# Kernel tuning notes

Hardware: AMD Instinct MI355X
Metric: run time of the kernel (lower is better)

Reference implementation:

```python
import jax, jax.numpy as jnp
import numpy as np

NUM_CLASSES = 80
STRIDES = (8, 16, 32)


def _decode(p, stride):
    # p: [B, 5+C, H, W] raw head -> [B, HW, 5+C] decoded (xy in px, wh=exp*stride)
    B, C, H, W = p.shape
    ys, xs = jnp.meshgrid(jnp.arange(H), jnp.arange(W), indexing='ij')
    grid = jnp.stack([xs, ys], -1).reshape(H * W, 2).astype(p.dtype)
    out = p.reshape(B, C, H * W).transpose(0, 2, 1)
    xy = (out[..., :2] + grid) * stride
    wh = jnp.exp(out[..., 2:4]) * stride
    out = jnp.concatenate([xy, wh, out[..., 4:]], -1)
    es = jnp.full((H * W,), float(stride), p.dtype)
    return out, grid[:, 0], grid[:, 1], es


def _pairwise_iou(gt, pr):
    # gt [G,4] cxcywh, pr [A,4] -> [G,A]
    gt_tl = gt[:, None, :2] - gt[:, None, 2:] * 0.5
    gt_br = gt[:, None, :2] + gt[:, None, 2:] * 0.5
    pr_tl = pr[None, :, :2] - pr[None, :, 2:] * 0.5
    pr_br = pr[None, :, :2] + pr[None, :, 2:] * 0.5
    tl = jnp.maximum(gt_tl, pr_tl)
    br = jnp.minimum(gt_br, pr_br)
    en = jnp.all(tl < br, -1).astype(gt.dtype)
    inter = jnp.prod(br - tl, -1) * en
    a_gt = jnp.prod(gt[:, 2:], -1)[:, None]
    a_pr = jnp.prod(pr[:, 2:], -1)[None, :]
    return inter / (a_gt + a_pr - inter + 1e-16)


def _assign(gt_boxes, gt_cls, bbox, clsp, objp, xg, yg, es):
    # SimOTA assignment for one image (all fixed-shape; non-candidate anchors
    # are masked out via huge cost instead of boolean gather).
    G = gt_boxes.shape[0]
    xc = (xg + 0.5) * es  # [A] anchor centers
    yc = (yg + 0.5) * es
    gl = gt_boxes[:, 0:1] - 0.5 * gt_boxes[:, 2:3]
    gr = gt_boxes[:, 0:1] + 0.5 * gt_boxes[:, 2:3]
    gt_ = gt_boxes[:, 1:2] - 0.5 * gt_boxes[:, 3:4]
    gb = gt_boxes[:, 1:2] + 0.5 * gt_boxes[:, 3:4]
    in_box = (xc[None] > gl) & (xc[None] < gr) & (yc[None] > gt_) & (yc[None] < gb)  # [G,A]
    r = 2.5 * es[None]
    in_ctr = ((xc[None] > gt_boxes[:, 0:1] - r) & (xc[None] < gt_boxes[:, 0:1] + r)
              & (yc[None] > gt_boxes[:, 1:2] - r) & (yc[None] < gt_boxes[:, 1:2] + r))
    fg_cand = jnp.any(in_box, 0) | jnp.any(in_ctr, 0)  # [A]
    in_both = in_box & in_ctr  # [G,A]

    ious = _pairwise_iou(gt_boxes, bbox)  # [G,A]
    ious_m = jnp.where(fg_cand[None, :], ious, 0.0)
    iou_cost = -jnp.log(ious_m + 1e-8)

    # pairwise cls BCE cost: bce(sqrt(sigmoid(cls)*sigmoid(obj)), onehot(gt)).sum(-1)
    p = jnp.sqrt(jax.nn.sigmoid(clsp) * jax.nn.sigmoid(objp[:, None]))  # [A,C]
    lp = jnp.maximum(jnp.log(p), -100.0)
    l1p = jnp.maximum(jnp.log1p(-p), -100.0)
    t = jax.nn.one_hot(gt_cls, NUM_CLASSES, dtype=p.dtype)  # [G,C]
    cls_cost = -(jnp.einsum('ac,gc->ga', lp - l1p, t) + jnp.sum(l1p, -1)[None, :])

    cost = (cls_cost + 3.0 * iou_cost
            + 1e5 * (~in_both).astype(p.dtype)
            + 1e9 * (~fg_cand)[None, :].astype(p.dtype))

    # dynamic-k: k_g = clamp(sum(top10 ious), min=1)
    topk_ious, _ = jax.lax.top_k(ious_m, 10)
    dyn_k = jnp.clip(topk_ious.sum(-1).astype(jnp.int32), 1, None)  # [G]
    rank = jnp.argsort(jnp.argsort(cost, axis=1), axis=1)  # rank of each anchor per gt
    matching = (rank < dyn_k[:, None]) & fg_cand[None, :]  # [G,A]
    # resolve anchors matched to multiple gts: keep min-cost gt
    multi = matching.sum(0) > 1
    best = jnp.argmin(cost, 0)
    matching = jnp.where(multi[None, :], jnp.arange(G)[:, None] == best[None, :], matching)

    fg = jnp.any(matching, 0)  # [A]
    matched_gt = jnp.argmax(matching, 0)  # [A]
    pred_iou = jnp.sum(matching * ious, 0)  # [A]
    matched_cls = gt_cls[matched_gt]
    return fg, matched_gt, pred_iou, matched_cls


def _giou_loss(b, g):
    tl = jnp.maximum(b[..., :2] - b[..., 2:] * 0.5, g[..., :2] - g[..., 2:] * 0.5)
    br = jnp.minimum(b[..., :2] + b[..., 2:] * 0.5, g[..., :2] + g[..., 2:] * 0.5)
    area_b = jnp.prod(b[..., 2:], -1)
    area_g = jnp.prod(g[..., 2:], -1)
    en = jnp.all(tl < br, -1).astype(b.dtype)
    inter = jnp.prod(br - tl, -1) * en
    union = area_b + area_g - inter
    iou = inter / (union + 1e-16)
    ctl = jnp.minimum(b[..., :2] - b[..., 2:] * 0.5, g[..., :2] - g[..., 2:] * 0.5)
    cbr = jnp.maximum(b[..., :2] + b[..., 2:] * 0.5, g[..., :2] + g[..., 2:] * 0.5)
    area_c = jnp.maximum(jnp.prod(cbr - ctl, -1), 1e-16)
    giou = iou - (area_c - union) / area_c
    return 1.0 - jnp.clip(giou, -1.0, 1.0)


def _bce_logits(x, t):
    return jnp.maximum(x, 0.0) - x * t + jnp.log1p(jnp.exp(-jnp.abs(x)))


def _forward(p8, p16, p32, labels):
    outs, xo, yo, eo = [], [], [], []
    for p, s in zip((p8, p16, p32), STRIDES):
        o, x, y, e = _decode(p, s)
        outs.append(o); xo.append(x); yo.append(y); eo.append(e)
    outputs = jnp.concatenate(outs, 1)  # [B, A, 5+C]
    xg = jnp.concatenate(xo); yg = jnp.concatenate(yo); es = jnp.concatenate(eo)

    bbox = outputs[..., :4]
    obj = outputs[..., 4]
    cls = outputs[..., 5:]
    gt_boxes = labels[..., :4]
    gt_cls = labels[..., 4].astype(jnp.int32)

    # assignment runs under no_grad in torch
    det = jax.lax.stop_gradient(outputs)
    fg, matched_gt, pred_iou, matched_cls = jax.vmap(
        lambda gb, gc, o: _assign(gb, gc, o[..., :4], o[..., 5:], o[..., 4], xg, yg, es)
    )(gt_boxes, gt_cls, det)

    fgf = fg.astype(outputs.dtype)  # [B,A]
    reg_t = jnp.take_along_axis(gt_boxes, matched_gt[..., None], axis=1)  # [B,A,4]
    cls_t = (jax.nn.one_hot(matched_cls, NUM_CLASSES, dtype=outputs.dtype)
             * pred_iou[..., None] * fgf[..., None])

    loss_iou = jnp.sum(_giou_loss(bbox, reg_t) * fgf)
    loss_obj = jnp.sum(_bce_logits(obj, fgf))
    loss_cls = jnp.sum(_bce_logits(cls, cls_t) * fgf[..., None])
    num_fg = jnp.maximum(jnp.sum(fgf), 1.0)
    return (5.0 * loss_iou + loss_obj + loss_cls) / num_fg


def setup_inputs() -> dict:
    key = jax.random.key(0)
    k1, k2, k3, k4, k5, k6 = jax.random.split(key, 6)
    B, NGT = 32, 20
    p8 = jax.random.normal(k1, (B, 5 + NUM_CLASSES, 80, 80), dtype=jnp.float32)
    p16 = jax.random.normal(k2, (B, 5 + NUM_CLASSES, 40, 40), dtype=jnp.float32)
    p32 = jax.random.normal(k3, (B, 5 + NUM_CLASSES, 20, 20), dtype=jnp.float32)
    cxy = jax.random.uniform(k4, (B, NGT, 2), dtype=jnp.float32, minval=32.0, maxval=608.0)
    wh = jax.random.uniform(k5, (B, NGT, 2), dtype=jnp.float32, minval=16.0, maxval=128.0)
    cls = jax.random.randint(k6, (B, NGT, 1), 0, NUM_CLASSES).astype(jnp.float32)
    labels = jnp.concatenate([cxy, wh, cls], -1)
    return {"p8": p8, "p16": p16, "p32": p32, "labels": labels}


def reference(p8, p16, p32, labels):
    return _forward(p8, p16, p32, labels)
```

## Files before the change

kernel.cpp:

```cpp
#include <hip/hip_runtime.h>
#include <cstdint>
#include <cstddef>

#define NA 8400
#define NAP 8448
#define NB 32
#define NG 20
#define NCL 80
#define NBLK 33

__device__ __forceinline__ float frcp(float x) { return __builtin_amdgcn_rcpf(x); }
__device__ __forceinline__ float bce0(float x) {
  return fmaxf(x, 0.0f) + __logf(1.0f + __expf(-fabsf(x)));
}

__device__ __forceinline__ void anchor_info(int a, const float* p8, const float* p16,
                                            const float* p32, int b, const float*& base,
                                            int& hw, int& HW, int& xg, int& yg, float& fs) {
  if (a < 6400)      { hw = a;        HW = 6400; xg = hw % 80; yg = hw / 80; fs = 8.f;
                       base = p8  + (size_t)b * 85 * 6400; }
  else if (a < 8000) { hw = a - 6400; HW = 1600; xg = hw % 40; yg = hw / 40; fs = 16.f;
                       base = p16 + (size_t)b * 85 * 1600; }
  else               { hw = a - 8000; HW = 400;  xg = hw % 20; yg = hw / 20; fs = 32.f;
                       base = p32 + (size_t)b * 85 * 400; }
}

__device__ __forceinline__ float iou_raw(float gx, float gy, float gw, float gh, float4 p) {
  float gtlx = gx - gw * 0.5f, gtly = gy - gh * 0.5f;
  float gbrx = gx + gw * 0.5f, gbry = gy + gh * 0.5f;
  float ptlx = p.x - p.z * 0.5f, ptly = p.y - p.w * 0.5f;
  float pbrx = p.x + p.z * 0.5f, pbry = p.y + p.w * 0.5f;
  float tlx = fmaxf(gtlx, ptlx), tly = fmaxf(gtly, ptly);
  float brx = fminf(gbrx, pbrx), bry = fminf(gbry, pbry);
  float inter = ((tlx < brx) && (tly < bry)) ? (brx - tlx) * (bry - tly) : 0.0f;
  float ag = gw * gh, ap = p.z * p.w;
  return inter * frcp(ag + ap - inter + 1e-16f);
}

__device__ __forceinline__ float cost_for(float gx, float gy, float gw, float gh, int cg,
                                          int g, unsigned int am, float lso, float slr,
                                          const float* base, int hw, int HW, float4 pb,
                                          float& iou_out) {
  float x = base[(size_t)(5 + cg) * HW + hw];
  float u = __logf(1.0f + __expf(-fabsf(x)));
  float lsx = fminf(x, 0.0f) - u;
  float lpr = 0.5f * (lsx + lso);
  float p   = __expf(lpr);
  float l1p = fmaxf(__logf(1.0f - p), -100.0f);
  float wv  = fmaxf(lpr, -100.0f) - l1p;
  float iou = iou_raw(gx, gy, gw, gh, pb);
  iou_out = iou;
  float cst = -(wv + slr) - 3.0f * __logf(iou + 1e-8f);
  if (!((am >> g) & 1u)) cst += 100000.0f;
  return cst;
}

__device__ __forceinline__ float giou_loss(float4 bb, float gx, float gy, float gw, float gh) {
  float btlx = bb.x - bb.z * 0.5f, btly = bb.y - bb.w * 0.5f;
  float bbrx = bb.x + bb.z * 0.5f, bbry = bb.y + bb.w * 0.5f;
  float gtlx = gx - gw * 0.5f, gtly = gy - gh * 0.5f;
  float gbrx = gx + gw * 0.5f, gbry = gy + gh * 0.5f;
  float tlx = fmaxf(btlx, gtlx), tly = fmaxf(btly, gtly);
  float brx = fminf(bbrx, gbrx), bry = fminf(bbry, gbry);
  float area_b = bb.z * bb.w, area_g = gw * gh;
  float inter = ((tlx < brx) && (tly < bry)) ? (brx - tlx) * (bry - tly) : 0.0f;
  float uni = area_b + area_g - inter;
  float iou = inter / (uni + 1e-16f);
  float ctlx = fminf(btlx, gtlx), ctly = fminf(btly, gtly);
  float cbrx = fmaxf(bbrx, gbrx), cbry = fmaxf(bbry, gbry);
  float area_c = fmaxf((cbrx - ctlx) * (cbry - ctly), 1e-16f);
  float giou = iou - (area_c - uni) / area_c;
  giou = fminf(fmaxf(giou, -1.0f), 1.0f);
  return 1.0f - giou;
}

__global__ __launch_bounds__(256) void kA(const float* __restrict__ p8,
                                          const float* __restrict__ p16,
                                          const float* __restrict__ p32,
                                          const float* __restrict__ labels,
                                          int* __restrict__ n_fg_cnt,
                                          float4* __restrict__ meta_c,
                                          float4* __restrict__ bbox_c,
                                          float* __restrict__ sb_c,
                                          unsigned int* __restrict__ match_c,
                                          float* __restrict__ blk_obj) {
  __shared__ float s_gt[NG * 4];
  __shared__ int   s_a[256];
  __shared__ unsigned int s_m[256];
  __shared__ float s_lso[256];
  __shared__ float s_sl[8][33];
  __shared__ float s_sbv[8][33];
  __shared__ unsigned int s_wcnt[4];
  __shared__ float s_part[4];
  __shared__ unsigned int s_base;
  __shared__ int s_cnt;

  int blk = blockIdx.x, b = blockIdx.y, tid = threadIdx.x, lane = tid & 63, wid = tid >> 6;
  size_t bo = (size_t)b * NAP;

  if (tid < NG) {
    s_gt[tid * 4 + 0] = labels[((size_t)b * NG + tid) * 5 + 0];
    s_gt[tid * 4 + 1] = labels[((size_t)b * NG + tid) * 5 + 1];
    s_gt[tid * 4 + 2] = labels[((size_t)b * NG + tid) * 5 + 2];
    s_gt[tid * 4 + 3] = labels[((size_t)b * NG + tid) * 5 + 3];
  }
  __syncthreads();

  int a = blk * 256 + tid;
  match_c[bo + a] = 0u;
  bool fg = false;
  unsigned int msk = 0u;
  float bce_obj = 0.0f, obj = 0.0f;
  const float* base = nullptr; int hw = 0, HW = 0, xg = 0, yg = 0; float fs = 8.f;
  if (a < NA) {
    anchor_info(a, p8, p16, p32, b, base, hw, HW, xg, yg, fs);
    obj = base[4 * HW + hw];
    bce_obj = bce0(obj);
    float xc = ((float)xg + 0.5f) * fs;
    float yc = ((float)yg + 0.5f) * fs;
    float r = 2.5f * fs;
#pragma unroll
    for (int g = 0; g < NG; ++g) {
      float gx = s_gt[g * 4 + 0], gy = s_gt[g * 4 + 1];
      float gw = s_gt[g * 4 + 2], gh = s_gt[g * 4 + 3];
      bool inb = (xc > gx - 0.5f * gw) && (xc < gx + 0.5f * gw) &&
                 (yc > gy - 0.5f * gh) && (yc < gy + 0.5f * gh);
      bool inc = (xc > gx - r) && (xc < gx + r) && (yc > gy - r) && (yc < gy + r);
      fg = fg || inb || inc;
      if (inb && inc) msk |= (1u << g);
    }
  }

  unsigned long long bm = __ballot(fg);
#pragma unroll
  for (int off = 32; off; off >>= 1) bce_obj += __shfl_down(bce_obj, off, 64);
  if (lane == 0) { s_wcnt[wid] = (unsigned int)__popcll(bm); s_part[wid] = bce_obj; }
  __syncthreads();
  if (tid == 0) {
    unsigned int cnt = s_wcnt[0] + s_wcnt[1] + s_wcnt[2] + s_wcnt[3];
    s_cnt = (int)cnt;
    s_base = cnt ? (unsigned int)atomicAdd(&n_fg_cnt[b], (int)cnt) : 0u;
    blk_obj[b * NBLK + blk] = s_part[0] + s_part[1] + s_part[2] + s_part[3];
  }
  __syncthreads();

  if (fg) {
    unsigned int li = 0;
    for (int w = 0; w < wid; ++w) li += s_wcnt[w];
    li += (unsigned int)__popcll(bm & ((1ull << lane) - 1ull));
    float v0 = base[hw];
    float v1 = base[HW + hw];
    float v2 = base[2 * HW + hw];
    float v3 = base[3 * HW + hw];
    float4 bb4 = make_float4((v0 + (float)xg) * fs, (v1 + (float)yg) * fs,
                             __expf(v2) * fs, __expf(v3) * fs);
    float uo = __logf(1.0f + __expf(-fabsf(obj)));
    float lso = fminf(obj, 0.0f) - uo;
    s_a[li] = a; s_m[li] = msk; s_lso[li] = lso;
    bbox_c[bo + s_base + li] = bb4;
  }
  __syncthreads();

  int cnt = s_cnt;
  int part = tid >> 5, cl = tid & 31;
  for (int t0 = 0; t0 < cnt; t0 += 32) {
    int idx = t0 + cl;
    bool act = idx < cnt;
    float sl = 0.0f, sb = 0.0f;
    if (act) {
      int a2 = s_a[idx];
      float lso = s_lso[idx];
      const float* base2; int hw2, HW2, xg2, yg2; float fs2;
      anchor_info(a2, p8, p16, p32, b, base2, hw2, HW2, xg2, yg2, fs2);
      const float* cb = base2 + (size_t)(5 + part * 10) * HW2 + hw2;
      float xs[10];
#pragma unroll
      for (int j = 0; j < 10; ++j) xs[j] = cb[(size_t)j * HW2];
#pragma unroll
      for (int j = 0; j < 10; ++j) {
        float x = xs[j];
        float u = __logf(1.0f + __expf(-fabsf(x)));
        sb += fmaxf(x, 0.0f) + u;
        float lsx = fminf(x, 0.0f) - u;
        float lpr = 0.5f * (lsx + lso);
        float p   = __expf(lpr);
        sl += fmaxf(__logf(1.0f - p), -100.0f);
      }
    }
    s_sl[part][cl] = sl;
    s_sbv[part][cl] = sb;
    __syncthreads();
    if (tid < 32) {
      int idx2 = t0 + tid;
      if (idx2 < cnt) {
        float tsl = 0.0f, tsb = 0.0f;
#pragma unroll
        for (int q = 0; q < 8; ++q) { tsl += s_sl[q][tid]; tsb += s_sbv[q][tid]; }
        int ci = (int)s_base + idx2;
        sb_c[bo + ci] = tsb;
        meta_c[bo + ci] = make_float4(s_lso[idx2], tsl,
                                      __uint_as_float(s_m[idx2]),
                                      __int_as_float(s_a[idx2]));
      }
    }
    __syncthreads();
  }
}

__global__ __launch_bounds__(256) void kBG(const float* __restrict__ p8,
                                           const float* __restrict__ p16,
                                           const float* __restrict__ p32,
                                           const float* __restrict__ labels,
                                           const int* __restrict__ n_fg,
                                           const float4* __restrict__ meta_c,
                                           const float4* __restrict__ bbox_c,
                                           const float* __restrict__ sb_c,
                                           unsigned int* __restrict__ match_c,
                                           const float* __restrict__ blk_obj,
                                           float* __restrict__ accum,
                                           int* __restrict__ done_g,
                                           int* __restrict__ done_img,
                                           float* __restrict__ out) {
  __shared__ float s_gt[NG * 5];
  __shared__ float s_wt[4 * 10];
  __shared__ float s_wc[4 * 10];
  __shared__ int   s_wi[4 * 10];
  __shared__ float s_red[16];
  __shared__ int   s_flag;

  int g = blockIdx.x, b = blockIdx.y, tid = threadIdx.x;
  int lane = tid & 63, wid = tid >> 6;
  int n = n_fg[b];
  size_t bo = (size_t)b * NAP;

  if (tid < NG * 5) s_gt[tid] = labels[(size_t)b * NG * 5 + tid];
  __syncthreads();

  float ggx = s_gt[g * 5], ggy = s_gt[g * 5 + 1];
  float ggw = s_gt[g * 5 + 2], ggh = s_gt[g * 5 + 3];
  int   gcg = (int)s_gt[g * 5 + 4];

  float t10[10];
  float c10v[10];
  int   c10i[10];
#pragma unroll
  for (int j = 0; j < 10; ++j) { t10[j] = 0.0f; c10v[j] = 3.4e38f; c10i[j] = 0x7fffffff; }

  for (int ci = tid; ci < n; ci += 256) {
    float4 me = meta_c[bo + ci];
    float lso = me.x, slr = me.y;
    unsigned int am = __float_as_uint(me.z);
    int a = __float_as_int(me.w);
    const float* base; int hw, HW, xg, yg; float fs;
    anchor_info(a, p8, p16, p32, b, base, hw, HW, xg, yg, fs);
    float4 pb = bbox_c[bo + ci];
    float iou;
    float cst = cost_for(ggx, ggy, ggw, ggh, gcg, g, am, lso, slr, base, hw, HW, pb, iou);
    if (iou > t10[9]) {
      t10[9] = iou;
#pragma unroll
      for (int q = 9; q > 0; --q) {
        if (t10[q] > t10[q - 1]) { float t = t10[q]; t10[q] = t10[q - 1]; t10[q - 1] = t; }
        else break;
      }
    }
    if (cst < c10v[9] || (cst == c10v[9] && ci < c10i[9])) {
      c10v[9] = cst; c10i[9] = ci;
#pragma unroll
      for (int q = 9; q > 0; --q) {
        if (c10v[q] < c10v[q - 1] ||
            (c10v[q] == c10v[q - 1] && c10i[q] < c10i[q - 1])) {
          float tv = c10v[q]; c10v[q] = c10v[q - 1]; c10v[q - 1] = tv;
          int   ti = c10i[q]; c10i[q] = c10i[q - 1]; c10i[q - 1] = ti;
        } else break;
      }
    }
  }

  for (int r = 0; r < 10; ++r) {
    float v = t10[0];
    float bv = v;
    float cv = c10v[0]; int cix = c10i[0];
    float cbv = cv;     int cbi = cix;
#pragma unroll
    for (int off = 32; off; off >>= 1) {
      bv = fmaxf(bv, __shfl_down(bv, off, 64));
      float ov = __shfl_down(cbv, off, 64);
      int   oi = __shfl_down(cbi, off, 64);
      if (ov < cbv || (ov == cbv && oi < cbi)) { cbv = ov; cbi = oi; }
    }
    bv  = __shfl(bv, 0, 64);
    cbv = __shfl(cbv, 0, 64);
    cbi = __shfl(cbi, 0, 64);
    unsigned long long won = __ballot(v == bv);
    if (lane == __ffsll(won) - 1) {
#pragma unroll
      for (int q = 0; q < 9; ++q) t10[q] = t10[q + 1];
      t10[9] = -1.0f;
    }
    if (cv == cbv && cix == cbi) {
#pragma unroll
      for (int q = 0; q < 9; ++q) { c10v[q] = c10v[q + 1]; c10i[q] = c10i[q + 1]; }
      c10v[9] = 3.4e38f; c10i[9] = 0x7fffffff;
    }
    if (lane == 0) {
      s_wt[wid * 10 + r] = bv;
      s_wc[wid * 10 + r] = cbv;
      s_wi[wid * 10 + r] = cbi;
    }
  }
  __syncthreads();

  if (tid == 0) {
    int p0 = 0, p1 = 0, p2 = 0, p3 = 0;
    float s = 0.0f;
    for (int r = 0; r < 10; ++r) {
      float v0 = (p0 < 10) ? s_wt[p0]      : -2.0f;
      float v1 = (p1 < 10) ? s_wt[10 + p1] : -2.0f;
      float v2 = (p2 < 10) ? s_wt[20 + p2] : -2.0f;
      float v3 = (p3 < 10) ? s_wt[30 + p3] : -2.0f;
      float m = fmaxf(fmaxf(v0, v1), fmaxf(v2, v3));
      s += m;
      if (m == v0) ++p0; else if (m == v1) ++p1; else if (m == v2) ++p2; else ++p3;
    }
    int k = (int)s;
    if (k < 1) k = 1;
    int q[4] = {0, 0, 0, 0};
    for (int it = 0; it < k; ++it) {
      float bv = 3.3e38f; int bi = 0x7fffffff; int sel = -1;
#pragma unroll
      for (int w = 0; w < 4; ++w) {
        if (q[w] < 10) {
          float v = s_wc[w * 10 + q[w]];
          int   i = s_wi[w * 10 + q[w]];
          if (v < bv || (v == bv && i < bi)) { bv = v; bi = i; sel = w; }
        }
      }
      if (sel < 0 || bv >= 1e37f) break;
      atomicOr(&match_c[bo + bi], 1u << g);
      ++q[sel];
    }
    __threadfence();
    s_flag = (atomicAdd(&done_g[b], 1) == NG - 1) ? 1 : 0;
  }
  __syncthreads();
  if (!s_flag) return;

  float li = 0.0f, oe = 0.0f, lc = 0.0f, nf = 0.0f;
  for (int ci = tid; ci < n; ci += 256) {
    unsigned int m = atomicOr(&match_c[bo + ci], 0u);
    if (m == 0u) continue;
    float4 me = meta_c[bo + ci];
    float lso = me.x, slr = me.y;
    unsigned int am = __float_as_uint(me.z);
    int a = __float_as_int(me.w);
    const float* base; int hw, HW, xg, yg; float fs;
    anchor_info(a, p8, p16, p32, b, base, hw, HW, xg, yg, fs);
    float4 pb = bbox_c[bo + ci];
    int mg;
    if (m & (m - 1)) {
      float bestc = 3.4e38f; mg = 0;
      for (int gq = 0; gq < NG; ++gq) {
        float iouq;
        float cq = cost_for(s_gt[gq * 5], s_gt[gq * 5 + 1], s_gt[gq * 5 + 2],
                            s_gt[gq * 5 + 3], (int)s_gt[gq * 5 + 4], gq, am,
                            lso, slr, base, hw, HW, pb, iouq);
        if (cq < bestc) { bestc = cq; mg = gq; }
      }
    } else {
      mg = __ffs(m) - 1;
    }
    float gx = s_gt[mg * 5], gy = s_gt[mg * 5 + 1];
    float gw = s_gt[mg * 5 + 2], gh = s_gt[mg * 5 + 3];
    int cgq = (int)s_gt[mg * 5 + 4];
    float piou = iou_raw(gx, gy, gw, gh, pb);
    li += giou_loss(pb, gx, gy, gw, gh);
    float xcls = base[(size_t)(5 + cgq) * HW + hw];
    lc += sb_c[bo + ci] - xcls * piou;
    oe += base[4 * HW + hw];
    nf += 1.0f;
  }

  float vals[4] = {li, oe, lc, nf};
#pragma unroll
  for (int q2 = 0; q2 < 4; ++q2) {
#pragma unroll
    for (int off = 32; off; off >>= 1) vals[q2] += __shfl_down(vals[q2], off, 64);
  }
  if (lane == 0) {
    s_red[wid * 4 + 0] = vals[0];
    s_red[wid * 4 + 1] = vals[1];
    s_red[wid * 4 + 2] = vals[2];
    s_red[wid * 4 + 3] = vals[3];
  }
  __syncthreads();
  if (tid < 4) {
    const int slot[4] = {0, 2, 3, 4};
    float s = s_red[tid] + s_red[4 + tid] + s_red[8 + tid] + s_red[12 + tid];
    atomicAdd(&accum[slot[tid]], s);
  }

  if (tid == 0) {
    __threadfence();
    s_flag = (atomicAdd(done_img, 1) == NB - 1) ? 1 : 0;
  }
  __syncthreads();
  if (!s_flag) return;

  float s = 0.0f;
  for (int i = tid; i < NB * NBLK; i += 256) s += blk_obj[i];
#pragma unroll
  for (int off = 32; off; off >>= 1) s += __shfl_down(s, off, 64);
  if ((tid & 63) == 0) s_red[tid >> 6] = s;
  __syncthreads();
  if (tid == 0) {
    float obj_base = s_red[0] + s_red[1] + s_red[2] + s_red[3];
    float loss_iou = atomicAdd(&accum[0], 0.0f);
    float oex      = atomicAdd(&accum[2], 0.0f);
    float loss_cls = atomicAdd(&accum[3], 0.0f);
    float num_fg   = atomicAdd(&accum[4], 0.0f);
    float loss_obj = obj_base - oex;
    out[0] = (5.0f * loss_iou + loss_obj + loss_cls) / fmaxf(num_fg, 1.0f);
  }
}

extern "C" void kernel_launch(void* const* d_in, const int* in_sizes, int n_in,
                              void* d_out, int out_size, void* d_ws, size_t ws_size,
                              hipStream_t stream) {
  const float* p8     = (const float*)d_in[0];
  const float* p16    = (const float*)d_in[1];
  const float* p32    = (const float*)d_in[2];
  const float* labels = (const float*)d_in[3];
  float* out = (float*)d_out;

  const size_t BAP = (size_t)NB * NAP;
  char* w = (char*)d_ws;
  float4*       bbox_c   = (float4*)w;
  float4*       meta_c   = (float4*)(w + BAP * 16);
  char*         w2       = w + BAP * 32;
  float*        sb_c     = (float*)(w2);
  unsigned int* match_c  = (unsigned int*)(w2 + BAP * 4);
  char*         w3       = w2 + BAP * 8;
  int*          n_fg     = (int*)w3;
  float*        accum    = (float*)(w3 + 128);
  int*          done_g   = (int*)(w3 + 256);
  int*          done_img = (int*)(w3 + 384);
  float*        blk_obj  = (float*)(w3 + 512);

  hipMemsetAsync(w3, 0, 512, stream);

  kA <<<dim3(NBLK, NB), dim3(256), 0, stream>>>(p8, p16, p32, labels, n_fg, meta_c,
                                                bbox_c, sb_c, match_c, blk_obj);
  kBG<<<dim3(NG, NB), dim3(256), 0, stream>>>(p8, p16, p32, labels, n_fg, meta_c, bbox_c,
                                              sb_c, match_c, blk_obj, accum, done_g,
                                              done_img, out);
}
```

Measured before the change: 188.3 us.

## Precompute per-GT class logits into compact table; simplify per-anchor class BCE pass

kA now computes the per-candidate class BCE sums in a single thread per anchor over all 80 classes, replacing the cooperative 8-way split with shared-memory reduction. It also writes a dense per-GT table of the gathered class logits and stores the objectness logit in meta. kBG then reads these compact arrays instead of doing strided gathers into the raw prediction tensors, which removes its scattered loads. In exchange, kA does more serial work per thread and writes an extra table of NB*NG*NAP floats.

```diff
diff --git a/kernel.cpp b/kernel.cpp
--- a/kernel.cpp
+++ b/kernel.cpp
@@ -37,11 +37,10 @@
   return inter * frcp(ag + ap - inter + 1e-16f);
 }
 
-__device__ __forceinline__ float cost_for(float gx, float gy, float gw, float gh, int cg,
-                                          int g, unsigned int am, float lso, float slr,
-                                          const float* base, int hw, int HW, float4 pb,
-                                          float& iou_out) {
-  float x = base[(size_t)(5 + cg) * HW + hw];
+__device__ __forceinline__ float cost_from_x(float x, float lso, float slr,
+                                             unsigned int am, int g,
+                                             float gx, float gy, float gw, float gh,
+                                             float4 pb, float& iou_out) {
   float u = __logf(1.0f + __expf(-fabsf(x)));
   float lsx = fminf(x, 0.0f) - u;
   float lpr = 0.5f * (lsx + lso);
@@ -82,18 +81,14 @@
                                           float4* __restrict__ meta_c,
                                           float4* __restrict__ bbox_c,
                                           float* __restrict__ sb_c,
+                                          float* __restrict__ x_tbl,
                                           unsigned int* __restrict__ match_c,
                                           float* __restrict__ blk_obj) {
   __shared__ float s_gt[NG * 4];
-  __shared__ int   s_a[256];
-  __shared__ unsigned int s_m[256];
-  __shared__ float s_lso[256];
-  __shared__ float s_sl[8][33];
-  __shared__ float s_sbv[8][33];
+  __shared__ int   s_gcls[NG];
   __shared__ unsigned int s_wcnt[4];
   __shared__ float s_part[4];
   __shared__ unsigned int s_base;
-  __shared__ int s_cnt;
 
   int blk = blockIdx.x, b = blockIdx.y, tid = threadIdx.x, lane = tid & 63, wid = tid >> 6;
   size_t bo = (size_t)b * NAP;
@@ -103,6 +98,7 @@
     s_gt[tid * 4 + 1] = labels[((size_t)b * NG + tid) * 5 + 1];
     s_gt[tid * 4 + 2] = labels[((size_t)b * NG + tid) * 5 + 2];
     s_gt[tid * 4 + 3] = labels[((size_t)b * NG + tid) * 5 + 3];
+    s_gcls[tid] = (int)labels[((size_t)b * NG + tid) * 5 + 4];
   }
   __syncthreads();
 
@@ -138,83 +134,56 @@
   __syncthreads();
   if (tid == 0) {
     unsigned int cnt = s_wcnt[0] + s_wcnt[1] + s_wcnt[2] + s_wcnt[3];
-    s_cnt = (int)cnt;
     s_base = cnt ? (unsigned int)atomicAdd(&n_fg_cnt[b], (int)cnt) : 0u;
     blk_obj[b * NBLK + blk] = s_part[0] + s_part[1] + s_part[2] + s_part[3];
   }
   __syncthreads();
 
-  if (fg) {
-    unsigned int li = 0;
-    for (int w = 0; w < wid; ++w) li += s_wcnt[w];
-    li += (unsigned int)__popcll(bm & ((1ull << lane) - 1ull));
-    float v0 = base[hw];
-    float v1 = base[HW + hw];
-    float v2 = base[2 * HW + hw];
-    float v3 = base[3 * HW + hw];
-    float4 bb4 = make_float4((v0 + (float)xg) * fs, (v1 + (float)yg) * fs,
-                             __expf(v2) * fs, __expf(v3) * fs);
-    float uo = __logf(1.0f + __expf(-fabsf(obj)));
-    float lso = fminf(obj, 0.0f) - uo;
-    s_a[li] = a; s_m[li] = msk; s_lso[li] = lso;
-    bbox_c[bo + s_base + li] = bb4;
-  }
-  __syncthreads();
-
-  int cnt = s_cnt;
-  int part = tid >> 5, cl = tid & 31;
-  for (int t0 = 0; t0 < cnt; t0 += 32) {
-    int idx = t0 + cl;
-    bool act = idx < cnt;
-    float sl = 0.0f, sb = 0.0f;
-    if (act) {
-      int a2 = s_a[idx];
-      float lso = s_lso[idx];
-      const float* base2; int hw2, HW2, xg2, yg2; float fs2;
-      anchor_info(a2, p8, p16, p32, b, base2, hw2, HW2, xg2, yg2, fs2);
-      const float* cb = base2 + (size_t)(5 + part * 10) * HW2 + hw2;
-      float xs[10];
-#pragma unroll
-      for (int j = 0; j < 10; ++j) xs[j] = cb[(size_t)j * HW2];
-#pragma unroll
-      for (int j = 0; j < 10; ++j) {
-        float x = xs[j];
-        float u = __logf(1.0f + __expf(-fabsf(x)));
-        sb += fmaxf(x, 0.0f) + u;
-        float lsx = fminf(x, 0.0f) - u;
-        float lpr = 0.5f * (lsx + lso);
-        float p   = __expf(lpr);
-        sl += fmaxf(__logf(1.0f - p), -100.0f);
-      }
-    }
-    s_sl[part][cl] = sl;
-    s_sbv[part][cl] = sb;
-    __syncthreads();
-    if (tid < 32) {
-      int idx2 = t0 + tid;
-      if (idx2 < cnt) {
-        float tsl = 0.0f, tsb = 0.0f;
-#pragma unroll
-        for (int q = 0; q < 8; ++q) { tsl += s_sl[q][tid]; tsb += s_sbv[q][tid]; }
-        int ci = (int)s_base + idx2;
-        sb_c[bo + ci] = tsb;
-        meta_c[bo + ci] = make_float4(s_lso[idx2], tsl,
-                                      __uint_as_float(s_m[idx2]),
-                                      __int_as_float(s_a[idx2]));
-      }
-    }
-    __syncthreads();
-  }
-}
-
-__global__ __launch_bounds__(256) void kBG(const float* __restrict__ p8,
-                                           const float* __restrict__ p16,
-                                           const float* __restrict__ p32,
-                                           const float* __restrict__ labels,
+  if (!fg) return;
+
+  unsigned int li = 0;
+  for (int w = 0; w < wid; ++w) li += s_wcnt[w];
+  li += (unsigned int)__popcll(bm & ((1ull << lane) - 1ull));
+  int ci = (int)(s_base + li);
+
+  float v0 = base[hw];
+  float v1 = base[HW + hw];
+  float v2 = base[2 * HW + hw];
+  float v3 = base[3 * HW + hw];
+  float4 bb4 = make_float4((v0 + (float)xg) * fs, (v1 + (float)yg) * fs,
+                           __expf(v2) * fs, __expf(v3) * fs);
+  float uo = __logf(1.0f + __expf(-fabsf(obj)));
+  float lso = fminf(obj, 0.0f) - uo;
+
+  float sb = 0.0f, sl = 0.0f;
+  const float* cb = base + (size_t)5 * HW + hw;
+  for (int c = 0; c < NCL; ++c) {
+    float x = cb[(size_t)c * HW];
+    float u = __logf(1.0f + __expf(-fabsf(x)));
+    sb += fmaxf(x, 0.0f) + u;
+    float lsx = fminf(x, 0.0f) - u;
+    float lpr = 0.5f * (lsx + lso);
+    float p   = __expf(lpr);
+    sl += fmaxf(__logf(1.0f - p), -100.0f);
+  }
+
+#pragma unroll
+  for (int g = 0; g < NG; ++g) {
+    float xgl = base[(size_t)(5 + s_gcls[g]) * HW + hw];
+    x_tbl[((size_t)b * NG + g) * NAP + ci] = xgl;
+  }
+
+  bbox_c[bo + ci] = bb4;
+  sb_c[bo + ci] = sb;
+  meta_c[bo + ci] = make_float4(lso, sl, __uint_as_float(msk), obj);
+}
+
+__global__ __launch_bounds__(256) void kBG(const float* __restrict__ labels,
                                            const int* __restrict__ n_fg,
                                            const float4* __restrict__ meta_c,
                                            const float4* __restrict__ bbox_c,
                                            const float* __restrict__ sb_c,
+                                           const float* __restrict__ x_tbl,
                                            unsigned int* __restrict__ match_c,
                                            const float* __restrict__ blk_obj,
                                            float* __restrict__ accum,
@@ -232,13 +201,13 @@
   int lane = tid & 63, wid = tid >> 6;
   int n = n_fg[b];
   size_t bo = (size_t)b * NAP;
+  const float* __restrict__ xrow = x_tbl + ((size_t)b * NG + g) * NAP;
 
   if (tid < NG * 5) s_gt[tid] = labels[(size_t)b * NG * 5 + tid];
   __syncthreads();
 
   float ggx = s_gt[g * 5], ggy = s_gt[g * 5 + 1];
   float ggw = s_gt[g * 5 + 2], ggh = s_gt[g * 5 + 3];
-  int   gcg = (int)s_gt[g * 5 + 4];
 
   float t10[10];
   float c10v[10];
@@ -248,14 +217,11 @@
 
   for (int ci = tid; ci < n; ci += 256) {
     float4 me = meta_c[bo + ci];
-    float lso = me.x, slr = me.y;
+    float4 pb = bbox_c[bo + ci];
+    float x = xrow[ci];
     unsigned int am = __float_as_uint(me.z);
-    int a = __float_as_int(me.w);
-    const float* base; int hw, HW, xg, yg; float fs;
-    anchor_info(a, p8, p16, p32, b, base, hw, HW, xg, yg, fs);
-    float4 pb = bbox_c[bo + ci];
     float iou;
-    float cst = cost_for(ggx, ggy, ggw, ggh, gcg, g, am, lso, slr, base, hw, HW, pb, iou);
+    float cst = cost_from_x(x, me.x, me.y, am, g, ggx, ggy, ggw, ggh, pb, iou);
     if (iou > t10[9]) {
       t10[9] = iou;
 #pragma unroll
@@ -351,20 +317,16 @@
     unsigned int m = atomicOr(&match_c[bo + ci], 0u);
     if (m == 0u) continue;
     float4 me = meta_c[bo + ci];
-    float lso = me.x, slr = me.y;
+    float4 pb = bbox_c[bo + ci];
     unsigned int am = __float_as_uint(me.z);
-    int a = __float_as_int(me.w);
-    const float* base; int hw, HW, xg, yg; float fs;
-    anchor_info(a, p8, p16, p32, b, base, hw, HW, xg, yg, fs);
-    float4 pb = bbox_c[bo + ci];
     int mg;
     if (m & (m - 1)) {
       float bestc = 3.4e38f; mg = 0;
       for (int gq = 0; gq < NG; ++gq) {
+        float xq = x_tbl[((size_t)b * NG + gq) * NAP + ci];
         float iouq;
-        float cq = cost_for(s_gt[gq * 5], s_gt[gq * 5 + 1], s_gt[gq * 5 + 2],
-                            s_gt[gq * 5 + 3], (int)s_gt[gq * 5 + 4], gq, am,
-                            lso, slr, base, hw, HW, pb, iouq);
+        float cq = cost_from_x(xq, me.x, me.y, am, gq, s_gt[gq * 5], s_gt[gq * 5 + 1],
+                               s_gt[gq * 5 + 2], s_gt[gq * 5 + 3], pb, iouq);
         if (cq < bestc) { bestc = cq; mg = gq; }
       }
     } else {
@@ -372,12 +334,11 @@
     }
     float gx = s_gt[mg * 5], gy = s_gt[mg * 5 + 1];
     float gw = s_gt[mg * 5 + 2], gh = s_gt[mg * 5 + 3];
-    int cgq = (int)s_gt[mg * 5 + 4];
     float piou = iou_raw(gx, gy, gw, gh, pb);
     li += giou_loss(pb, gx, gy, gw, gh);
-    float xcls = base[(size_t)(5 + cgq) * HW + hw];
+    float xcls = x_tbl[((size_t)b * NG + mg) * NAP + ci];
     lc += sb_c[bo + ci] - xcls * piou;
-    oe += base[4 * HW + hw];
+    oe += me.w;
     nf += 1.0f;
   }
 
@@ -437,7 +398,8 @@
   char* w = (char*)d_ws;
   float4*       bbox_c   = (float4*)w;
   float4*       meta_c   = (float4*)(w + BAP * 16);
-  char*         w2       = w + BAP * 32;
+  float*        x_tbl    = (float*)(w + BAP * 32);
+  char*         w2       = (char*)x_tbl + (size_t)NB * NG * NAP * 4;
   float*        sb_c     = (float*)(w2);
   unsigned int* match_c  = (unsigned int*)(w2 + BAP * 4);
   char*         w3       = w2 + BAP * 8;
@@ -450,8 +412,8 @@
   hipMemsetAsync(w3, 0, 512, stream);
 
   kA <<<dim3(NBLK, NB), dim3(256), 0, stream>>>(p8, p16, p32, labels, n_fg, meta_c,
-                                                bbox_c, sb_c, match_c, blk_obj);
-  kBG<<<dim3(NG, NB), dim3(256), 0, stream>>>(p8, p16, p32, labels, n_fg, meta_c, bbox_c,
-                                              sb_c, match_c, blk_obj, accum, done_g,
+                                                bbox_c, sb_c, x_tbl, match_c, blk_obj);
+  kBG<<<dim3(NG, NB), dim3(256), 0, stream>>>(labels, n_fg, meta_c, bbox_c, sb_c, x_tbl,
+                                              match_c, blk_obj, accum, done_g,
                                               done_img, out);
 }
```

New measurement: 208.4 us. +10.7%, slower.
